# Performance work log

Hardware: AMD Instinct MI355X
Metric: run time of the kernel (lower is better)

## Reference

```python
import jax, jax.numpy as jnp
import numpy as np

B, N, C, H, K = 2, 4096, 256, 8, 32
D = C // H
EPS = 1e-5


def _ln(x, w, b):
    # LayerNorm over last axis
    m = x.mean(-1, keepdims=True)
    v = x.var(-1, keepdims=True)
    return (x - m) * jax.lax.rsqrt(v + EPS) * w + b


def setup_inputs() -> dict:
    key = jax.random.key(0)
    ks = jax.random.split(key, 16)
    s = 1.0 / np.sqrt(C)
    inp = {
        'xyz_A': jax.random.normal(ks[0], (B, N, 3), jnp.float32),
        'xyz_B': jax.random.normal(ks[1], (B, N, 3), jnp.float32),
        'featA': jax.random.normal(ks[2], (B, C, N), jnp.float32),
        'featB': jax.random.normal(ks[3], (B, C, N), jnp.float32),
        'ln_in_w': jnp.ones((C,), jnp.float32), 'ln_in_b': jnp.zeros((C,), jnp.float32),
        'wq': jax.random.normal(ks[4], (C, C), jnp.float32) * s, 'bq': jnp.zeros((C,), jnp.float32),
        'wk': jax.random.normal(ks[5], (C, C), jnp.float32) * s, 'bk': jnp.zeros((C,), jnp.float32),
        'wv': jax.random.normal(ks[6], (C, C), jnp.float32) * s, 'bv': jnp.zeros((C,), jnp.float32),
        'wqd': jax.random.normal(ks[7], (C, C), jnp.float32) * s, 'bqd': jnp.zeros((C,), jnp.float32),
        'wkd': jax.random.normal(ks[8], (C, C), jnp.float32) * s, 'bkd': jnp.zeros((C,), jnp.float32),
        'ln_sim_w': jnp.ones((C,), jnp.float32), 'ln_sim_b': jnp.zeros((C,), jnp.float32),
        'ln_dis_w': jnp.ones((C,), jnp.float32), 'ln_dis_b': jnp.zeros((C,), jnp.float32),
        'fus_w1': jax.random.normal(ks[9], (2 * C, 3 * C), jnp.float32) * (1.0 / np.sqrt(3 * C)),
        'bn_g': jnp.ones((2 * C,), jnp.float32), 'bn_b': jnp.zeros((2 * C,), jnp.float32),
        'fus_w2': jax.random.normal(ks[10], (C, 2 * C), jnp.float32) * (1.0 / np.sqrt(2 * C)),
        'fus_b2': jnp.zeros((C,), jnp.float32),
    }
    return inp


def reference(xyz_A, xyz_B, featA, featB, ln_in_w, ln_in_b,
              wq, bq, wk, bk, wv, bv, wqd, bqd, wkd, bkd,
              ln_sim_w, ln_sim_b, ln_dis_w, ln_dis_b,
              fus_w1, bn_g, bn_b, fus_w2, fus_b2):
    xA = featA.transpose(0, 2, 1)   # (B,N,C)
    xB = featB.transpose(0, 2, 1)   # (B,N,C)
    xA_n = _ln(xA, ln_in_w, ln_in_b)

    # KNN: nearest K points of xyz_B for each point in xyz_A
    d2 = (jnp.sum(xyz_A * xyz_A, -1)[:, :, None]
          + jnp.sum(xyz_B * xyz_B, -1)[:, None, :]
          - 2.0 * jnp.einsum('bnc,bmc->bnm', xyz_A, xyz_B))  # (B,N,N)
    _, knn_idx = jax.lax.top_k(-d2, K)  # (B,N,K)

    def proj(x, W, b):  # Conv1d k=1 on (B,N,C)
        return jnp.einsum('bnc,oc->bno', x, W) + b

    def heads(x):
        return x.reshape(B, N, H, D)

    q_s = heads(proj(xA_n, wq, bq))
    k_s = heads(proj(xB, wk, bk))
    v = heads(proj(xB, wv, bv))

    gather = jax.vmap(lambda f, i: f[i])  # (N,H,D),(N,K) -> (N,K,H,D)
    kN = gather(k_s, knn_idx)   # (B,N,K,H,D)
    vN = gather(v, knn_idx)     # (B,N,K,H,D)

    # similarity path: scaled dot-product over K neighbors
    sim = jnp.einsum('bnhd,bnkhd->bnhk', q_s, kN) / jnp.sqrt(jnp.float32(D))
    w_sim = jax.nn.softmax(sim, -1)
    ctx_s = jnp.einsum('bnhk,bnkhd->bnhd', w_sim, vN).reshape(B, N, C)
    ctx_s = _ln(ctx_s, ln_sim_w, ln_sim_b)

    # dissimilarity path: L2 distance scores
    q_d = heads(proj(xA_n, wqd, bqd))
    k_d = heads(proj(xB, wkd, bkd))
    kdN = gather(k_d, knn_idx)  # (B,N,K,H,D)
    diff = q_d[:, :, None] - kdN
    dist = jnp.sqrt(jnp.sum(diff * diff, -1)).transpose(0, 1, 3, 2)  # (B,N,H,K)
    w_dis = jax.nn.softmax(dist, -1)
    ctx_d = jnp.einsum('bnhk,bnkhd->bnhd', w_dis, vN).reshape(B, N, C)
    ctx_d = _ln(ctx_d, ln_dis_w, ln_dis_b)

    # fusion MLP (BN in eval mode: running mean 0, var 1)
    fused = jnp.concatenate([xA_n, ctx_s, ctx_d], -1)  # (B,N,3C)
    y = jnp.einsum('bnc,oc->bno', fused, fus_w1)
    y = y * jax.lax.rsqrt(jnp.float32(1.0 + EPS)) * bn_g + bn_b
    y = jax.nn.relu(y)
    y = jnp.einsum('bnc,oc->bno', y, fus_w2) + fus_b2

    out = y + xA  # residual (identity since in_channel == out_channel)
    return out.transpose(0, 2, 1)  # (B,C,N)
```

## Files before the change

kernel.cpp:

```cpp
#include <hip/hip_runtime.h>
#include <hip/hip_bf16.h>
#include <math.h>

#define B_ 2
#define N_ 4096
#define C_ 256
#define H_ 8
#define K_ 32
#define NP_ (B_*N_)
#define CAPW 256

typedef __attribute__((ext_vector_type(8))) short bf16x8;
typedef __attribute__((ext_vector_type(4))) float f32x4;
typedef __attribute__((ext_vector_type(4))) unsigned short ushort4_t;

__device__ __forceinline__ float bf2f(unsigned short v){
    union { unsigned int u; float f; } x; x.u = ((unsigned int)v) << 16; return x.f;
}
__device__ __forceinline__ unsigned short f2bf(float f){
    union { float f; unsigned int u; } x; x.f = f;
    return (unsigned short)((x.u + 0x7FFFu + ((x.u >> 16) & 1u)) >> 16);
}
__device__ __forceinline__ unsigned int mono(float f){
    union { float f; unsigned int u; } x; x.f = f;
    return x.u ^ (0x80000000u | (unsigned int)((int)x.u >> 31));
}
__device__ __forceinline__ void gload_lds16(const unsigned short* g, unsigned short* l){
    __builtin_amdgcn_global_load_lds(
        (const __attribute__((address_space(1))) unsigned int*)g,
        (__attribute__((address_space(3))) unsigned int*)l, 16, 0, 0);
}

__global__ __launch_bounds__(256) void k_pre(
    const float* __restrict__ s0, const float* __restrict__ s1,
    const float* __restrict__ s2, const float* __restrict__ s3,
    const float* __restrict__ s4, const float* __restrict__ s5,
    const float* __restrict__ s6, unsigned short* __restrict__ Wb,
    const float* __restrict__ xyzB, f32x4* __restrict__ PB,
    const float* __restrict__ xyzA, int* __restrict__ order,
    const float* __restrict__ featA, const float* __restrict__ lnw,
    const float* __restrict__ lnb, unsigned short* __restrict__ F,
    const float* __restrict__ featB, unsigned short* __restrict__ XBT)
{
    __shared__ __align__(16) char smem[35200];
    const int bid = blockIdx.x;
    const int tid = threadIdx.x;
    if (bid < 832){
        int i = (bid*256 + tid)*4;
        const float* s; int off;
        if (i < 327680){
            int seg = i >> 16;
            s = (seg==0)?s0:(seg==1)?s1:(seg==2)?s2:(seg==3)?s3:s4;
            off = i & 65535;
        } else if (i < 720896){
            s = s5; off = i - 327680;
        } else {
            s = s6; off = i - 720896;
        }
        f32x4 v = *(const f32x4*)(s + off);
        ushort4_t o;
        #pragma unroll
        for (int e = 0; e < 4; e++) o[e] = f2bf(v[e]);
        *(ushort4_t*)(Wb + i) = o;
    } else if (bid < 864){
        int i = (bid - 832)*256 + tid;
        float x = xyzB[i*3], y = xyzB[i*3+1], z = xyzB[i*3+2];
        f32x4 o;
        o[0] = -2.f*x; o[1] = -2.f*y; o[2] = -2.f*z;
        o[3] = x*x + y*y + z*z;
        PB[i] = o;
    } else if (bid < 866){
        unsigned int* hist = (unsigned int*)smem;
        unsigned int* wsum = (unsigned int*)(smem + 4096);
        const int b = bid - 864;
        const int wv = tid >> 6, lane = tid & 63;
        for (int i = tid; i < 1024; i += 256) hist[i] = 0u;
        __syncthreads();
        unsigned int code[16];
        #pragma unroll
        for (int i = 0; i < 16; i++){
            const int n = tid + i*256;
            const float* pp = xyzA + (size_t)((b<<12) + n)*3;
            int qx = (int)fminf(fmaxf((pp[0] + 5.f)*1.6f, 0.f), 15.f);
            int qy = (int)fminf(fmaxf((pp[1] + 5.f)*0.8f, 0.f), 7.f);
            int qz = (int)fminf(fmaxf((pp[2] + 5.f)*0.8f, 0.f), 7.f);
            unsigned int c = (unsigned int)((qx & 1) | ((qz & 1) << 1) | ((qy & 1) << 2)
                           | (((qx >> 1) & 1) << 3) | (((qz >> 1) & 1) << 4) | (((qy >> 1) & 1) << 5)
                           | (((qx >> 2) & 1) << 6) | (((qz >> 2) & 1) << 7) | (((qy >> 2) & 1) << 8)
                           | (((qx >> 3) & 1) << 9));
            code[i] = c;
            atomicAdd(&hist[c], 1u);
        }
        __syncthreads();
        unsigned int loc[4], t4 = 0;
        #pragma unroll
        for (int j = 0; j < 4; j++){ loc[j] = hist[tid*4 + j]; t4 += loc[j]; }
        unsigned int sc = t4;
        #pragma unroll
        for (int off = 1; off < 64; off <<= 1){
            unsigned int o = __shfl_up(sc, off, 64);
            if (lane >= off) sc += o;
        }
        if (lane == 63) wsum[wv] = sc;
        __syncthreads();
        unsigned int wb = 0;
        #pragma unroll
        for (int j = 0; j < 4; j++) if (j < wv) wb += wsum[j];
        unsigned int base = wb + sc - t4;
        #pragma unroll
        for (int j = 0; j < 4; j++){ hist[tid*4 + j] = base; base += loc[j]; }
        __syncthreads();
        #pragma unroll
        for (int i = 0; i < 16; i++){
            const int n = tid + i*256;
            unsigned int pos = atomicAdd(&hist[code[i]], 1u);
            order[(b<<12) + pos] = (b<<12) | n;
        }
    } else if (bid < 1122){
        float (*tile)[257] = (float(*)[257])smem;
        float (*ps)[32]    = (float(*)[32])(smem + 32896);
        float (*pq)[32]    = (float(*)[32])(smem + 33920);
        float (*st)[32]    = (float(*)[32])(smem + 34944);
        const int nx = tid & 31, cy = tid >> 5;
        const int pbase = (bid - 866) * 32;
        const int b = pbase >> 12, n0 = pbase & 4095;
        const float* sp = featA + (size_t)b*C_*N_ + n0;
        #pragma unroll 4
        for (int it = 0; it < 32; it++){
            int c = cy + it*8;
            tile[nx][c] = sp[(size_t)c*N_ + nx];
        }
        __syncthreads();
        {
            float s = 0.f, q = 0.f;
            #pragma unroll 8
            for (int i = 0; i < 32; i++){
                int cc = cy*32 + ((i + cy) & 31);
                float x = tile[nx][cc];
                s += x; q = fmaf(x, x, q);
            }
            ps[cy][nx] = s; pq[cy][nx] = q;
        }
        __syncthreads();
        if (tid < 32){
            float S = 0.f, Q = 0.f;
            #pragma unroll
            for (int j = 0; j < 8; j++){ S += ps[j][tid]; Q += pq[j][tid]; }
            float m = S*(1.f/256.f);
            float v = Q*(1.f/256.f) - m*m;
            st[0][tid] = m; st[1][tid] = rsqrtf(v + 1e-5f);
        }
        __syncthreads();
        const int p = pbase + nx;
        const float m = st[0][nx], r = st[1][nx];
        #pragma unroll
        for (int j = 0; j < 4; j++){
            bf16x8 ob;
            #pragma unroll
            for (int e = 0; e < 8; e++){
                int c = cy*32 + j*8 + e;
                ob[e] = (short)f2bf((tile[nx][c]-m)*r*lnw[c] + lnb[c]);
            }
            *(bf16x8*)(F + (size_t)p*768 + cy*32 + j*8) = ob;
        }
    } else {
        float (*tile)[65] = (float(*)[65])smem;
        const int idx = bid - 1122;
        const int x = idx & 63, y = (idx >> 6) & 3, z = idx >> 8;
        const int n0 = x*64, c0 = y*64;
        const int tx = tid & 63, ty = tid >> 6;
        const float* sp = featB + (size_t)z*C_*N_;
        #pragma unroll
        for (int i = 0; i < 16; i++){
            int cr = ty + i*4;
            tile[cr][tx] = sp[(size_t)(c0+cr)*N_ + n0 + tx];
        }
        __syncthreads();
        const int c = c0 + tx;
        #pragma unroll
        for (int i = 0; i < 16; i++){
            int nr = ty + i*4;
            int p = (z<<12) + n0 + nr;
            XBT[(size_t)p*256 + c] = f2bf(tile[tx][nr]);
        }
    }
}

__global__ __launch_bounds__(256) void k_knn(const float* __restrict__ xyzA,
        const f32x4* __restrict__ PB, int* __restrict__ knn){
    const int wv = threadIdx.x >> 6, lane = threadIdx.x & 63;
    const int p = blockIdx.x*4 + wv;
    const int b = p >> 12;
    const f32x4* pb = PB + ((size_t)b << 12);
    const float ax = xyzA[(size_t)p*3], ay = xyzA[(size_t)p*3+1], az = xyzA[(size_t)p*3+2];

    unsigned long long mn = ~0ull;
    #pragma unroll 8
    for (int i = 0; i < 64; i++){
        const int m = i*64 + lane;
        f32x4 c = pb[m];
        float d = fmaf(ax, c[0], fmaf(ay, c[1], fmaf(az, c[2], c[3])));
        unsigned long long key = (((unsigned long long)mono(d)) << 12) | (unsigned int)m;
        mn = key < mn ? key : mn;
    }
    unsigned int rk = 0;
    for (int j = 0; j < 64; j++){
        unsigned long long o = __shfl(mn, j, 64);
        rk += (o < mn) ? 1u : 0u;
    }
    unsigned long long sel = (rk == 31u) ? mn : ~0ull;
    #pragma unroll
    for (int off = 32; off; off >>= 1){
        unsigned long long o = __shfl_xor(sel, off, 64);
        sel = o < sel ? o : sel;
    }
    const unsigned long long v = sel;
    const unsigned int vhi = (unsigned int)(v >> 12);
    const unsigned int vlo = (unsigned int)(v & 0xFFFull);

    __shared__ unsigned long long cand[4][CAPW];
    __shared__ unsigned int cnt[4];
    if (lane == 0) cnt[wv] = 0u;
    #pragma unroll 8
    for (int i = 0; i < 64; i++){
        const int m = i*64 + lane;
        f32x4 c = pb[m];
        float d = fmaf(ax, c[0], fmaf(ay, c[1], fmaf(az, c[2], c[3])));
        unsigned int u = mono(d);
        if (u < vhi || (u == vhi && (unsigned int)m <= vlo)){
            unsigned int slot = atomicAdd(&cnt[wv], 1u);
            if (slot < CAPW)
                cand[wv][slot] = (((unsigned long long)u) << 12) | (unsigned int)m;
        }
    }
    const unsigned int C = cnt[wv];
    if (C <= CAPW){
        for (unsigned int i = lane; i < C; i += 64){
            unsigned long long mk = cand[wv][i];
            unsigned int rank = 0;
            for (unsigned int j = 0; j < C; j++) rank += (cand[wv][j] < mk) ? 1u : 0u;
            if (rank < K_) knn[(size_t)p*K_ + rank] = (int)(mk & 0xFFFull);
        }
    } else {
        unsigned long long last = 0ull;
        for (int it = 0; it < K_; it++){
            unsigned long long cm = ~0ull;
            #pragma unroll 4
            for (int i = 0; i < 64; i++){
                const int m = i*64 + lane;
                f32x4 c = pb[m];
                float d = fmaf(ax, c[0], fmaf(ay, c[1], fmaf(az, c[2], c[3])));
                unsigned long long key = (((unsigned long long)mono(d)) << 12) | (unsigned int)m;
                if (key > last && key < cm) cm = key;
            }
            #pragma unroll
            for (int off = 32; off; off >>= 1){
                unsigned long long o = __shfl_xor(cm, off, 64);
                cm = o < cm ? o : cm;
            }
            if (lane == 0) knn[(size_t)p*K_ + it] = (int)(cm & 0xFFFull);
            last = cm;
        }
    }
}

template<int MODE>
__device__ __forceinline__ void gemm_body(
    const unsigned short* __restrict__ X, int ldx,
    const unsigned short* __restrict__ W, int Kin,
    const float* __restrict__ e0, const float* __restrict__ e1, const float* __restrict__ e2,
    unsigned short* __restrict__ Y, int ldy,
    const float* __restrict__ resid, float* __restrict__ out,
    unsigned short (*As)[128*32], unsigned short (*Bs)[64*32], int bx, int by)
{
    const int tid = threadIdx.x, wid = tid >> 6, lane = tid & 63;
    const int lr = lane & 15, lg = lane >> 4;
    const int m0 = bx*128, n0 = by*64;
    const int lrow = lane >> 2, lcol = (lane & 3)*8;

    const unsigned short* Ag0 = X + (size_t)(m0 + wid*32 + lrow)*ldx + lcol;
    const unsigned short* Ag1 = X + (size_t)(m0 + wid*32 + 16 + lrow)*ldx + lcol;
    const unsigned short* Bg0 = W + (size_t)(n0 + wid*16 + lrow)*Kin + lcol;

    f32x4 acc[2][4] = {};
    const int NT = Kin >> 5;
    int buf = 0;
    gload_lds16(Ag0, &As[0][(wid*32)*32]);
    gload_lds16(Ag1, &As[0][(wid*32+16)*32]);
    gload_lds16(Bg0, &Bs[0][(wid*16)*32]);
    __syncthreads();
    for (int kt = 0; kt < NT; kt++){
        if (kt + 1 < NT){
            const int k = (kt+1)*32;
            gload_lds16(Ag0 + k, &As[buf^1][(wid*32)*32]);
            gload_lds16(Ag1 + k, &As[buf^1][(wid*32+16)*32]);
            gload_lds16(Bg0 + k, &Bs[buf^1][(wid*16)*32]);
        }
        bf16x8 a[2], b[4];
        #pragma unroll
        for (int mi = 0; mi < 2; mi++)
            a[mi] = *(const bf16x8*)&As[buf][(wid*32 + mi*16 + lr)*32 + lg*8];
        #pragma unroll
        for (int ni = 0; ni < 4; ni++)
            b[ni] = *(const bf16x8*)&Bs[buf][(ni*16 + lr)*32 + lg*8];
        #pragma unroll
        for (int mi = 0; mi < 2; mi++){
            #pragma unroll
            for (int ni = 0; ni < 4; ni++)
                acc[mi][ni] = __builtin_amdgcn_mfma_f32_16x16x32_bf16(a[mi], b[ni], acc[mi][ni], 0, 0, 0);
        }
        __syncthreads();
        buf ^= 1;
    }
    #pragma unroll
    for (int mi = 0; mi < 2; mi++){
        const int pbase = m0 + wid*32 + mi*16 + lg*4;
        #pragma unroll
        for (int ni = 0; ni < 4; ni++){
            const int o = n0 + ni*16 + lr;
            if (MODE == 0){
                const float* bp = (o < 256) ? e0 : ((o < 512) ? e1 : e2);
                float bias = bp[o & 255];
                #pragma unroll
                for (int r = 0; r < 4; r++)
                    Y[(size_t)(pbase + r)*ldy + o] = f2bf(acc[mi][ni][r] + bias);
            } else if (MODE == 1){
                float sc = e0[o] * 0.9999950000374997f;
                float sh = e1[o];
                #pragma unroll
                for (int r = 0; r < 4; r++){
                    float vv = fmaf(acc[mi][ni][r], sc, sh);
                    Y[(size_t)(pbase + r)*ldy + o] = f2bf(fmaxf(vv, 0.f));
                }
            } else {
                float bias = e0[o];
                const int b = pbase >> 12, nn = pbase & 4095;
                const size_t adr = ((size_t)b*C_ + o)*N_ + nn;
                f32x4 rv = *(const f32x4*)(resid + adr);
                f32x4 ov;
                #pragma unroll
                for (int r = 0; r < 4; r++) ov[r] = acc[mi][ni][r] + bias + rv[r];
                *(f32x4*)(out + adr) = ov;
            }
        }
    }
}

__global__ __launch_bounds__(256) void k_proj(
    const unsigned short* __restrict__ F, const unsigned short* __restrict__ XBT,
    const unsigned short* __restrict__ WQcat, const unsigned short* __restrict__ WKVD,
    const float* __restrict__ bq, const float* __restrict__ bqd,
    const float* __restrict__ bk, const float* __restrict__ bv, const float* __restrict__ bkd,
    unsigned short* __restrict__ QQ, unsigned short* __restrict__ KVD)
{
    __shared__ __align__(16) unsigned short As[2][128*32];
    __shared__ __align__(16) unsigned short Bs[2][64*32];
    if (blockIdx.y < 8)
        gemm_body<0>(F, 768, WQcat, 256, bq, bqd, nullptr, QQ, 512, nullptr, nullptr,
                     As, Bs, blockIdx.x, blockIdx.y);
    else
        gemm_body<0>(XBT, 256, WKVD, 256, bk, bv, bkd, KVD, 768, nullptr, nullptr,
                     As, Bs, blockIdx.x, blockIdx.y - 8);
}

template<int MODE>
__global__ __launch_bounds__(256) void k_gemm(
    const unsigned short* __restrict__ X, int ldx,
    const unsigned short* __restrict__ W, int Kin,
    const float* __restrict__ e0, const float* __restrict__ e1, const float* __restrict__ e2,
    unsigned short* __restrict__ Y, int ldy,
    const float* __restrict__ resid, float* __restrict__ out)
{
    __shared__ __align__(16) unsigned short As[2][128*32];
    __shared__ __align__(16) unsigned short Bs[2][64*32];
    gemm_body<MODE>(X, ldx, W, Kin, e0, e1, e2, Y, ldy, resid, out,
                    As, Bs, blockIdx.x, blockIdx.y);
}

__global__ __launch_bounds__(128) void k_attn(
    const unsigned short* __restrict__ QQ, const unsigned short* __restrict__ KVD,
    const int* __restrict__ KNN, const int* __restrict__ order,
    const float* __restrict__ lnsw, const float* __restrict__ lnsb,
    const float* __restrict__ lndw, const float* __restrict__ lndb,
    unsigned short* __restrict__ F)
{
    __shared__ int   idx_l[2][32];
    __shared__ float part_l[2][4];

    const int tid = threadIdx.x;
    const int wh = tid >> 6, lane = tid & 63;
    const int bid = blockIdx.x;
    const int xcd = bid & 7, ib = bid >> 3;
    const int batch = xcd & 1, quarter = xcd >> 1;
    const int p = order[(batch << 12) + quarter*1024 + ib];
    const int b = batch;

    if (lane < 32) idx_l[wh][lane] = KNN[(size_t)p*K_ + lane];

    const int tq = lane >> 4, c = lane & 15;

    float qsf[8], qdf[8];
    {
        const unsigned short* qrow = QQ + (size_t)p*512 + wh*128 + c*8;
        bf16x8 qs8 = *(const bf16x8*)(qrow);
        bf16x8 qd8 = *(const bf16x8*)(qrow + 256);
        #pragma unroll
        for (int e = 0; e < 8; e++){
            qsf[e] = bf2f((unsigned short)qs8[e]);
            qdf[e] = bf2f((unsigned short)qd8[e]);
        }
    }
    const unsigned short* KB = KVD + (size_t)(b << 12)*768;
    int nbt[8];
    #pragma unroll
    for (int i = 0; i < 8; i++) nbt[i] = idx_l[wh][tq + i*4];

    float s[8];
    {
        bf16x8 kx[8];
        #pragma unroll
        for (int i = 0; i < 8; i++)
            kx[i] = *(const bf16x8*)(KB + (size_t)nbt[i]*768 + wh*128 + c*8);
        #pragma unroll
        for (int i = 0; i < 8; i++){
            float a = 0.f;
            #pragma unroll
            for (int e = 0; e < 8; e++)
                a = fmaf(qsf[e], bf2f((unsigned short)kx[i][e]), a);
            s[i] = a;
        }
    }
    float t[8];
    {
        bf16x8 dx[8];
        #pragma unroll
        for (int i = 0; i < 8; i++)
            dx[i] = *(const bf16x8*)(KB + (size_t)nbt[i]*768 + 512 + wh*128 + c*8);
        #pragma unroll
        for (int i = 0; i < 8; i++){
            float a = 0.f;
            #pragma unroll
            for (int e = 0; e < 8; e++){
                float df = qdf[e] - bf2f((unsigned short)dx[i][e]);
                a = fmaf(df, df, a);
            }
            t[i] = a;
        }
    }
    bf16x8 vx[8];
    #pragma unroll
    for (int i = 0; i < 8; i++)
        vx[i] = *(const bf16x8*)(KB + (size_t)nbt[i]*768 + 256 + wh*128 + c*8);

    #pragma unroll
    for (int i = 0; i < 8; i++){
        s[i] += __shfl_xor(s[i], 1, 64); s[i] += __shfl_xor(s[i], 2, 64);
        t[i] += __shfl_xor(t[i], 1, 64); t[i] += __shfl_xor(t[i], 2, 64);
    }
    float sim[8], dist[8];
    #pragma unroll
    for (int i = 0; i < 8; i++){
        sim[i]  = s[i] * 0.17677669529663687f;
        dist[i] = sqrtf(t[i]);
    }
    float m1 = sim[0], m2 = dist[0];
    #pragma unroll
    for (int i = 1; i < 8; i++){ m1 = fmaxf(m1, sim[i]); m2 = fmaxf(m2, dist[i]); }
    m1 = fmaxf(m1, __shfl_xor(m1, 16, 64)); m1 = fmaxf(m1, __shfl_xor(m1, 32, 64));
    m2 = fmaxf(m2, __shfl_xor(m2, 16, 64)); m2 = fmaxf(m2, __shfl_xor(m2, 32, 64));
    float e1[8], e2[8], s1 = 0.f, s2 = 0.f;
    #pragma unroll
    for (int i = 0; i < 8; i++){
        e1[i] = __expf(sim[i] - m1);  s1 += e1[i];
        e2[i] = __expf(dist[i] - m2); s2 += e2[i];
    }
    s1 += __shfl_xor(s1, 16, 64); s1 += __shfl_xor(s1, 32, 64);
    s2 += __shfl_xor(s2, 16, 64); s2 += __shfl_xor(s2, 32, 64);
    const float r1i = 1.f / s1, r2i = 1.f / s2;

    float cs[8] = {0,0,0,0,0,0,0,0}, cd[8] = {0,0,0,0,0,0,0,0};
    #pragma unroll
    for (int i = 0; i < 8; i++){
        const float w1 = e1[i] * r1i;
        const float w2 = e2[i] * r2i;
        #pragma unroll
        for (int e = 0; e < 8; e++){
            float vf = bf2f((unsigned short)vx[i][e]);
            cs[e] = fmaf(w1, vf, cs[e]);
            cd[e] = fmaf(w2, vf, cd[e]);
        }
    }
    #pragma unroll
    for (int e = 0; e < 8; e++){
        cs[e] += __shfl_xor(cs[e], 16, 64); cs[e] += __shfl_xor(cs[e], 32, 64);
        cd[e] += __shfl_xor(cd[e], 16, 64); cd[e] += __shfl_xor(cd[e], 32, 64);
    }
    float s1n = 0.f, q1n = 0.f, s2n = 0.f, q2n = 0.f;
    #pragma unroll
    for (int e = 0; e < 8; e++){
        s1n += cs[e]; q1n = fmaf(cs[e], cs[e], q1n);
        s2n += cd[e]; q2n = fmaf(cd[e], cd[e], q2n);
    }
    #pragma unroll
    for (int off = 1; off < 16; off <<= 1){
        s1n += __shfl_xor(s1n, off, 64); q1n += __shfl_xor(q1n, off, 64);
        s2n += __shfl_xor(s2n, off, 64); q2n += __shfl_xor(q2n, off, 64);
    }
    if (lane == 0){
        part_l[wh][0] = s1n; part_l[wh][1] = q1n;
        part_l[wh][2] = s2n; part_l[wh][3] = q2n;
    }
    __syncthreads();
    const float S1 = s1n + part_l[wh^1][0];
    const float Q1 = q1n + part_l[wh^1][1];
    const float S2 = s2n + part_l[wh^1][2];
    const float Q2 = q2n + part_l[wh^1][3];
    const float mm1 = S1*(1.f/256.f), mm2 = S2*(1.f/256.f);
    const float rr1 = rsqrtf(Q1*(1.f/256.f) - mm1*mm1 + 1e-5f);
    const float rr2 = rsqrtf(Q2*(1.f/256.f) - mm2*mm2 + 1e-5f);

    if (tq == 0){
        bf16x8 ob;
        #pragma unroll
        for (int e = 0; e < 8; e++){
            const int cg = wh*128 + c*8 + e;
            ob[e] = (short)f2bf((cs[e]-mm1)*rr1*lnsw[cg] + lnsb[cg]);
        }
        *(bf16x8*)(F + (size_t)p*768 + 256 + wh*128 + c*8) = ob;
    } else if (tq == 1){
        bf16x8 ob;
        #pragma unroll
        for (int e = 0; e < 8; e++){
            const int cg = wh*128 + c*8 + e;
            ob[e] = (short)f2bf((cd[e]-mm2)*rr2*lndw[cg] + lndb[cg]);
        }
        *(bf16x8*)(F + (size_t)p*768 + 512 + wh*128 + c*8) = ob;
    }
}

extern "C" void kernel_launch(void* const* d_in, const int* in_sizes, int n_in,
                              void* d_out, int out_size, void* d_ws, size_t ws_size,
                              hipStream_t stream)
{
    const float* xyzA   = (const float*)d_in[0];
    const float* xyzB   = (const float*)d_in[1];
    const float* featA  = (const float*)d_in[2];
    const float* featB  = (const float*)d_in[3];
    const float* ln_in_w= (const float*)d_in[4];
    const float* ln_in_b= (const float*)d_in[5];
    const float* wq  = (const float*)d_in[6];
    const float* bq  = (const float*)d_in[7];
    const float* wk  = (const float*)d_in[8];
    const float* bk  = (const float*)d_in[9];
    const float* wv  = (const float*)d_in[10];
    const float* bv  = (const float*)d_in[11];
    const float* wqd = (const float*)d_in[12];
    const float* bqd = (const float*)d_in[13];
    const float* wkd = (const float*)d_in[14];
    const float* bkd = (const float*)d_in[15];
    const float* lnsw = (const float*)d_in[16];
    const float* lnsb = (const float*)d_in[17];
    const float* lndw = (const float*)d_in[18];
    const float* lndb = (const float*)d_in[19];
    const float* fw1 = (const float*)d_in[20];
    const float* bng = (const float*)d_in[21];
    const float* bnb = (const float*)d_in[22];
    const float* fw2 = (const float*)d_in[23];
    const float* fb2 = (const float*)d_in[24];
    float* out = (float*)d_out;
    char* ws = (char*)d_ws;

    unsigned short* F    = (unsigned short*)(ws + 0);
    unsigned short* XBT  = (unsigned short*)(ws + 12582912);
    unsigned short* QQ   = (unsigned short*)(ws + 16777216);
    unsigned short* KVD  = (unsigned short*)(ws + 25165824);
    unsigned short* Y1   = (unsigned short*)(ws + 37748736);
    f32x4*          PB   = (f32x4*)(ws + 37748736);
    int*            KNNi = (int*)(ws + 46137344);
    int*            ORD  = (int*)(ws + 47185920);
    unsigned short* Wb   = (unsigned short*)(ws + 47251456);
    unsigned short* WQcat = Wb;
    unsigned short* WKVD  = Wb + 131072;
    unsigned short* W1b   = Wb + 327680;
    unsigned short* W2b   = Wb + 720896;

    k_pre<<<1634, 256, 0, stream>>>(wq, wqd, wk, wv, wkd, fw1, fw2, Wb,
                                    xyzB, PB, xyzA, ORD,
                                    featA, ln_in_w, ln_in_b, F, featB, XBT);
    k_knn<<<2048, 256, 0, stream>>>(xyzA, PB, KNNi);

    k_proj<<<dim3(64,20), 256, 0, stream>>>(F, XBT, WQcat, WKVD, bq, bqd, bk, bv, bkd, QQ, KVD);

    k_attn<<<8192, 128, 0, stream>>>(QQ, KVD, KNNi, ORD, lnsw, lnsb, lndw, lndb, F);

    k_gemm<1><<<dim3(64,8), 256, 0, stream>>>(F,  768, W1b, 768, bng, bnb, nullptr, Y1, 512, nullptr, nullptr);
    k_gemm<2><<<dim3(64,4), 256, 0, stream>>>(Y1, 512, W2b, 512, fb2, nullptr, nullptr, nullptr, 0, featA, out);
}
```

Baseline: 129.1 us.

## Process two query points per wavefront in KNN to reuse candidate loads

The KNN kernel now has each wavefront handle two query points, so every loaded B-point coordinate feeds two distance computations and the grid is halved. The first min pass tracks float distance plus index instead of packed 64-bit keys, and the candidate filter compares floats against an unmono'd threshold. This cuts global loads and 64-bit compares per query. In exchange it doubles shared candidate storage, adds register pressure, and changes how ties at the threshold are handled, which can let more candidates through the filter.

After: 127.9 us. Within noise of the previous version (-0.9%).

```diff
diff --git a/kernel.cpp b/kernel.cpp
--- a/kernel.cpp
+++ b/kernel.cpp
@@ -24,6 +24,11 @@
 __device__ __forceinline__ unsigned int mono(float f){
     union { float f; unsigned int u; } x; x.f = f;
     return x.u ^ (0x80000000u | (unsigned int)((int)x.u >> 31));
+}
+__device__ __forceinline__ float unmono(unsigned int u){
+    union { unsigned int u; float f; } x;
+    x.u = (u & 0x80000000u) ? (u ^ 0x80000000u) : ~u;
+    return x.f;
 }
 __device__ __forceinline__ void gload_lds16(const unsigned short* g, unsigned short* l){
     __builtin_amdgcn_global_load_lds(
@@ -189,77 +194,125 @@
 __global__ __launch_bounds__(256) void k_knn(const float* __restrict__ xyzA,
         const f32x4* __restrict__ PB, int* __restrict__ knn){
     const int wv = threadIdx.x >> 6, lane = threadIdx.x & 63;
-    const int p = blockIdx.x*4 + wv;
-    const int b = p >> 12;
+    const int q0 = blockIdx.x*8 + wv*2;
+    const int b = q0 >> 12;
     const f32x4* pb = PB + ((size_t)b << 12);
-    const float ax = xyzA[(size_t)p*3], ay = xyzA[(size_t)p*3+1], az = xyzA[(size_t)p*3+2];
-
-    unsigned long long mn = ~0ull;
+    const float ax0 = xyzA[(size_t)q0*3],     ay0 = xyzA[(size_t)q0*3+1],     az0 = xyzA[(size_t)q0*3+2];
+    const float ax1 = xyzA[(size_t)(q0+1)*3], ay1 = xyzA[(size_t)(q0+1)*3+1], az1 = xyzA[(size_t)(q0+1)*3+2];
+
+    float dm0 = 3.4e38f, dm1 = 3.4e38f;
+    int   mi0 = 0, mi1 = 0;
     #pragma unroll 8
     for (int i = 0; i < 64; i++){
         const int m = i*64 + lane;
         f32x4 c = pb[m];
-        float d = fmaf(ax, c[0], fmaf(ay, c[1], fmaf(az, c[2], c[3])));
-        unsigned long long key = (((unsigned long long)mono(d)) << 12) | (unsigned int)m;
-        mn = key < mn ? key : mn;
-    }
-    unsigned int rk = 0;
+        float d0 = fmaf(ax0, c[0], fmaf(ay0, c[1], fmaf(az0, c[2], c[3])));
+        float d1 = fmaf(ax1, c[0], fmaf(ay1, c[1], fmaf(az1, c[2], c[3])));
+        if (d0 < dm0){ dm0 = d0; mi0 = m; }
+        if (d1 < dm1){ dm1 = d1; mi1 = m; }
+    }
+    const unsigned long long key0 = (((unsigned long long)mono(dm0)) << 12) | (unsigned int)mi0;
+    const unsigned long long key1 = (((unsigned long long)mono(dm1)) << 12) | (unsigned int)mi1;
+    unsigned int rk0 = 0, rk1 = 0;
     for (int j = 0; j < 64; j++){
-        unsigned long long o = __shfl(mn, j, 64);
-        rk += (o < mn) ? 1u : 0u;
-    }
-    unsigned long long sel = (rk == 31u) ? mn : ~0ull;
+        unsigned long long o0 = __shfl(key0, j, 64);
+        unsigned long long o1 = __shfl(key1, j, 64);
+        rk0 += (o0 < key0) ? 1u : 0u;
+        rk1 += (o1 < key1) ? 1u : 0u;
+    }
+    unsigned long long sel0 = (rk0 == 31u) ? key0 : ~0ull;
+    unsigned long long sel1 = (rk1 == 31u) ? key1 : ~0ull;
     #pragma unroll
     for (int off = 32; off; off >>= 1){
-        unsigned long long o = __shfl_xor(sel, off, 64);
-        sel = o < sel ? o : sel;
-    }
-    const unsigned long long v = sel;
-    const unsigned int vhi = (unsigned int)(v >> 12);
-    const unsigned int vlo = (unsigned int)(v & 0xFFFull);
-
-    __shared__ unsigned long long cand[4][CAPW];
-    __shared__ unsigned int cnt[4];
-    if (lane == 0) cnt[wv] = 0u;
-    #pragma unroll 8
+        unsigned long long o0 = __shfl_xor(sel0, off, 64);
+        unsigned long long o1 = __shfl_xor(sel1, off, 64);
+        sel0 = o0 < sel0 ? o0 : sel0;
+        sel1 = o1 < sel1 ? o1 : sel1;
+    }
+    const float vf0 = unmono((unsigned int)(sel0 >> 12));
+    const float vf1 = unmono((unsigned int)(sel1 >> 12));
+
+    __shared__ unsigned long long cand[8][CAPW];
+    __shared__ unsigned int cnt[8];
+    const int s0 = wv*2, s1 = wv*2 + 1;
+    if (lane == 0){ cnt[s0] = 0u; cnt[s1] = 0u; }
+    #pragma unroll 4
     for (int i = 0; i < 64; i++){
         const int m = i*64 + lane;
         f32x4 c = pb[m];
-        float d = fmaf(ax, c[0], fmaf(ay, c[1], fmaf(az, c[2], c[3])));
-        unsigned int u = mono(d);
-        if (u < vhi || (u == vhi && (unsigned int)m <= vlo)){
-            unsigned int slot = atomicAdd(&cnt[wv], 1u);
+        float d0 = fmaf(ax0, c[0], fmaf(ay0, c[1], fmaf(az0, c[2], c[3])));
+        float d1 = fmaf(ax1, c[0], fmaf(ay1, c[1], fmaf(az1, c[2], c[3])));
+        if (d0 <= vf0){
+            unsigned int slot = atomicAdd(&cnt[s0], 1u);
             if (slot < CAPW)
-                cand[wv][slot] = (((unsigned long long)u) << 12) | (unsigned int)m;
-        }
-    }
-    const unsigned int C = cnt[wv];
-    if (C <= CAPW){
-        for (unsigned int i = lane; i < C; i += 64){
-            unsigned long long mk = cand[wv][i];
-            unsigned int rank = 0;
-            for (unsigned int j = 0; j < C; j++) rank += (cand[wv][j] < mk) ? 1u : 0u;
-            if (rank < K_) knn[(size_t)p*K_ + rank] = (int)(mk & 0xFFFull);
-        }
-    } else {
-        unsigned long long last = 0ull;
-        for (int it = 0; it < K_; it++){
-            unsigned long long cm = ~0ull;
-            #pragma unroll 4
-            for (int i = 0; i < 64; i++){
-                const int m = i*64 + lane;
-                f32x4 c = pb[m];
-                float d = fmaf(ax, c[0], fmaf(ay, c[1], fmaf(az, c[2], c[3])));
-                unsigned long long key = (((unsigned long long)mono(d)) << 12) | (unsigned int)m;
-                if (key > last && key < cm) cm = key;
-            }
-            #pragma unroll
-            for (int off = 32; off; off >>= 1){
-                unsigned long long o = __shfl_xor(cm, off, 64);
-                cm = o < cm ? o : cm;
-            }
-            if (lane == 0) knn[(size_t)p*K_ + it] = (int)(cm & 0xFFFull);
-            last = cm;
+                cand[s0][slot] = (((unsigned long long)mono(d0)) << 12) | (unsigned int)m;
+        }
+        if (d1 <= vf1){
+            unsigned int slot = atomicAdd(&cnt[s1], 1u);
+            if (slot < CAPW)
+                cand[s1][slot] = (((unsigned long long)mono(d1)) << 12) | (unsigned int)m;
+        }
+    }
+    {
+        const unsigned int C = cnt[s0];
+        if (C <= CAPW){
+            for (unsigned int i = lane; i < C; i += 64){
+                unsigned long long mk = cand[s0][i];
+                unsigned int rank = 0;
+                for (unsigned int j = 0; j < C; j++) rank += (cand[s0][j] < mk) ? 1u : 0u;
+                if (rank < K_) knn[(size_t)q0*K_ + rank] = (int)(mk & 0xFFFull);
+            }
+        } else {
+            unsigned long long last = 0ull;
+            for (int it = 0; it < K_; it++){
+                unsigned long long cm = ~0ull;
+                #pragma unroll 4
+                for (int i = 0; i < 64; i++){
+                    const int m = i*64 + lane;
+                    f32x4 c = pb[m];
+                    float d = fmaf(ax0, c[0], fmaf(ay0, c[1], fmaf(az0, c[2], c[3])));
+                    unsigned long long key = (((unsigned long long)mono(d)) << 12) | (unsigned int)m;
+                    if (key > last && key < cm) cm = key;
+                }
+                #pragma unroll
+                for (int off = 32; off; off >>= 1){
+                    unsigned long long o = __shfl_xor(cm, off, 64);
+                    cm = o < cm ? o : cm;
+                }
+                if (lane == 0) knn[(size_t)q0*K_ + it] = (int)(cm & 0xFFFull);
+                last = cm;
+            }
+        }
+    }
+    {
+        const unsigned int C = cnt[s1];
+        if (C <= CAPW){
+            for (unsigned int i = lane; i < C; i += 64){
+                unsigned long long mk = cand[s1][i];
+                unsigned int rank = 0;
+                for (unsigned int j = 0; j < C; j++) rank += (cand[s1][j] < mk) ? 1u : 0u;
+                if (rank < K_) knn[(size_t)(q0+1)*K_ + rank] = (int)(mk & 0xFFFull);
+            }
+        } else {
+            unsigned long long last = 0ull;
+            for (int it = 0; it < K_; it++){
+                unsigned long long cm = ~0ull;
+                #pragma unroll 4
+                for (int i = 0; i < 64; i++){
+                    const int m = i*64 + lane;
+                    f32x4 c = pb[m];
+                    float d = fmaf(ax1, c[0], fmaf(ay1, c[1], fmaf(az1, c[2], c[3])));
+                    unsigned long long key = (((unsigned long long)mono(d)) << 12) | (unsigned int)m;
+                    if (key > last && key < cm) cm = key;
+                }
+                #pragma unroll
+                for (int off = 32; off; off >>= 1){
+                    unsigned long long o = __shfl_xor(cm, off, 64);
+                    cm = o < cm ? o : cm;
+                }
+                if (lane == 0) knn[(size_t)(q0+1)*K_ + it] = (int)(cm & 0xFFFull);
+                last = cm;
+            }
         }
     }
 }
@@ -587,7 +640,7 @@
     k_pre<<<1634, 256, 0, stream>>>(wq, wqd, wk, wv, wkd, fw1, fw2, Wb,
                                     xyzB, PB, xyzA, ORD,
                                     featA, ln_in_w, ln_in_b, F, featB, XBT);
-    k_knn<<<2048, 256, 0, stream>>>(xyzA, PB, KNNi);
+    k_knn<<<1024, 256, 0, stream>>>(xyzA, PB, KNNi);
 
     k_proj<<<dim3(64,20), 256, 0, stream>>>(F, XBT, WQcat, WKVD, bq, bqd, bk, bv, bkd, QQ, KVD);
 
```

## Process four query points per wavefront in KNN to reuse loaded candidates

Applied to the files above, without the earlier changes.

Each wavefront of the KNN kernel now handles four query points, so every candidate point loaded from global memory is reused for four distance evaluations. The grid shrinks from 2048 to 512 blocks and the shared candidate buffer becomes 16 slabs with capacity cut from 256 to 128. The threshold filter now compares float distances against an un-mapped threshold instead of packed integer keys. The risks are fewer blocks in flight (less latency hiding), more register pressure, and more frequent fallback to the slow iterative path if a candidate list overflows 128.

Measured after the change: 138.5 us. 7.3% more time.

```diff
diff --git a/kernel.cpp b/kernel.cpp
--- a/kernel.cpp
+++ b/kernel.cpp
@@ -8,7 +8,7 @@
 #define H_ 8
 #define K_ 32
 #define NP_ (B_*N_)
-#define CAPW 256
+#define CAPW 128
 
 typedef __attribute__((ext_vector_type(8))) short bf16x8;
 typedef __attribute__((ext_vector_type(4))) float f32x4;
@@ -24,6 +24,11 @@
 __device__ __forceinline__ unsigned int mono(float f){
     union { float f; unsigned int u; } x; x.f = f;
     return x.u ^ (0x80000000u | (unsigned int)((int)x.u >> 31));
+}
+__device__ __forceinline__ float unmono(unsigned int u){
+    union { unsigned int u; float f; } x;
+    x.u = (u & 0x80000000u) ? (u ^ 0x80000000u) : ~u;
+    return x.f;
 }
 __device__ __forceinline__ void gload_lds16(const unsigned short* g, unsigned short* l){
     __builtin_amdgcn_global_load_lds(
@@ -189,77 +194,104 @@
 __global__ __launch_bounds__(256) void k_knn(const float* __restrict__ xyzA,
         const f32x4* __restrict__ PB, int* __restrict__ knn){
     const int wv = threadIdx.x >> 6, lane = threadIdx.x & 63;
-    const int p = blockIdx.x*4 + wv;
-    const int b = p >> 12;
+    const int q0 = blockIdx.x*16 + wv*4;
+    const int b = q0 >> 12;
     const f32x4* pb = PB + ((size_t)b << 12);
-    const float ax = xyzA[(size_t)p*3], ay = xyzA[(size_t)p*3+1], az = xyzA[(size_t)p*3+2];
-
-    unsigned long long mn = ~0ull;
-    #pragma unroll 8
+    float axq[4], ayq[4], azq[4];
+    #pragma unroll
+    for (int qq = 0; qq < 4; qq++){
+        axq[qq] = xyzA[(size_t)(q0+qq)*3];
+        ayq[qq] = xyzA[(size_t)(q0+qq)*3+1];
+        azq[qq] = xyzA[(size_t)(q0+qq)*3+2];
+    }
+
+    float dm[4] = {3.4e38f, 3.4e38f, 3.4e38f, 3.4e38f};
+    int   mi[4] = {0,0,0,0};
+    #pragma unroll 4
     for (int i = 0; i < 64; i++){
         const int m = i*64 + lane;
         f32x4 c = pb[m];
-        float d = fmaf(ax, c[0], fmaf(ay, c[1], fmaf(az, c[2], c[3])));
-        unsigned long long key = (((unsigned long long)mono(d)) << 12) | (unsigned int)m;
-        mn = key < mn ? key : mn;
-    }
-    unsigned int rk = 0;
+        #pragma unroll
+        for (int qq = 0; qq < 4; qq++){
+            float d = fmaf(axq[qq], c[0], fmaf(ayq[qq], c[1], fmaf(azq[qq], c[2], c[3])));
+            if (d < dm[qq]){ dm[qq] = d; mi[qq] = m; }
+        }
+    }
+    unsigned long long key[4];
+    #pragma unroll
+    for (int qq = 0; qq < 4; qq++)
+        key[qq] = (((unsigned long long)mono(dm[qq])) << 12) | (unsigned int)mi[qq];
+    unsigned int rk[4] = {0,0,0,0};
     for (int j = 0; j < 64; j++){
-        unsigned long long o = __shfl(mn, j, 64);
-        rk += (o < mn) ? 1u : 0u;
-    }
-    unsigned long long sel = (rk == 31u) ? mn : ~0ull;
+        #pragma unroll
+        for (int qq = 0; qq < 4; qq++){
+            unsigned long long o = __shfl(key[qq], j, 64);
+            rk[qq] += (o < key[qq]) ? 1u : 0u;
+        }
+    }
+    unsigned long long sel[4];
+    #pragma unroll
+    for (int qq = 0; qq < 4; qq++) sel[qq] = (rk[qq] == 31u) ? key[qq] : ~0ull;
     #pragma unroll
     for (int off = 32; off; off >>= 1){
-        unsigned long long o = __shfl_xor(sel, off, 64);
-        sel = o < sel ? o : sel;
-    }
-    const unsigned long long v = sel;
-    const unsigned int vhi = (unsigned int)(v >> 12);
-    const unsigned int vlo = (unsigned int)(v & 0xFFFull);
-
-    __shared__ unsigned long long cand[4][CAPW];
-    __shared__ unsigned int cnt[4];
-    if (lane == 0) cnt[wv] = 0u;
-    #pragma unroll 8
+        #pragma unroll
+        for (int qq = 0; qq < 4; qq++){
+            unsigned long long o = __shfl_xor(sel[qq], off, 64);
+            sel[qq] = o < sel[qq] ? o : sel[qq];
+        }
+    }
+    float vf[4];
+    #pragma unroll
+    for (int qq = 0; qq < 4; qq++) vf[qq] = unmono((unsigned int)(sel[qq] >> 12));
+
+    __shared__ unsigned long long cand[16][CAPW];
+    __shared__ unsigned int cnt[16];
+    if (lane < 4) cnt[wv*4 + lane] = 0u;
+    #pragma unroll 4
     for (int i = 0; i < 64; i++){
         const int m = i*64 + lane;
         f32x4 c = pb[m];
-        float d = fmaf(ax, c[0], fmaf(ay, c[1], fmaf(az, c[2], c[3])));
-        unsigned int u = mono(d);
-        if (u < vhi || (u == vhi && (unsigned int)m <= vlo)){
-            unsigned int slot = atomicAdd(&cnt[wv], 1u);
-            if (slot < CAPW)
-                cand[wv][slot] = (((unsigned long long)u) << 12) | (unsigned int)m;
-        }
-    }
-    const unsigned int C = cnt[wv];
-    if (C <= CAPW){
-        for (unsigned int i = lane; i < C; i += 64){
-            unsigned long long mk = cand[wv][i];
-            unsigned int rank = 0;
-            for (unsigned int j = 0; j < C; j++) rank += (cand[wv][j] < mk) ? 1u : 0u;
-            if (rank < K_) knn[(size_t)p*K_ + rank] = (int)(mk & 0xFFFull);
-        }
-    } else {
-        unsigned long long last = 0ull;
-        for (int it = 0; it < K_; it++){
-            unsigned long long cm = ~0ull;
-            #pragma unroll 4
-            for (int i = 0; i < 64; i++){
-                const int m = i*64 + lane;
-                f32x4 c = pb[m];
-                float d = fmaf(ax, c[0], fmaf(ay, c[1], fmaf(az, c[2], c[3])));
-                unsigned long long key = (((unsigned long long)mono(d)) << 12) | (unsigned int)m;
-                if (key > last && key < cm) cm = key;
+        #pragma unroll
+        for (int qq = 0; qq < 4; qq++){
+            float d = fmaf(axq[qq], c[0], fmaf(ayq[qq], c[1], fmaf(azq[qq], c[2], c[3])));
+            if (d <= vf[qq]){
+                unsigned int slot = atomicAdd(&cnt[wv*4 + qq], 1u);
+                if (slot < CAPW)
+                    cand[wv*4 + qq][slot] = (((unsigned long long)mono(d)) << 12) | (unsigned int)m;
             }
-            #pragma unroll
-            for (int off = 32; off; off >>= 1){
-                unsigned long long o = __shfl_xor(cm, off, 64);
-                cm = o < cm ? o : cm;
+        }
+    }
+    #pragma unroll
+    for (int qq = 0; qq < 4; qq++){
+        const int slab = wv*4 + qq;
+        const unsigned int C = cnt[slab];
+        if (C <= CAPW){
+            for (unsigned int i = lane; i < C; i += 64){
+                unsigned long long mk = cand[slab][i];
+                unsigned int rank = 0;
+                for (unsigned int j = 0; j < C; j++) rank += (cand[slab][j] < mk) ? 1u : 0u;
+                if (rank < K_) knn[(size_t)(q0+qq)*K_ + rank] = (int)(mk & 0xFFFull);
             }
-            if (lane == 0) knn[(size_t)p*K_ + it] = (int)(cm & 0xFFFull);
-            last = cm;
+        } else {
+            unsigned long long last = 0ull;
+            for (int it = 0; it < K_; it++){
+                unsigned long long cm = ~0ull;
+                #pragma unroll 4
+                for (int i = 0; i < 64; i++){
+                    const int m = i*64 + lane;
+                    f32x4 c = pb[m];
+                    float d = fmaf(axq[qq], c[0], fmaf(ayq[qq], c[1], fmaf(azq[qq], c[2], c[3])));
+                    unsigned long long kk2 = (((unsigned long long)mono(d)) << 12) | (unsigned int)m;
+                    if (kk2 > last && kk2 < cm) cm = kk2;
+                }
+                #pragma unroll
+                for (int off = 32; off; off >>= 1){
+                    unsigned long long o = __shfl_xor(cm, off, 64);
+                    cm = o < cm ? o : cm;
+                }
+                if (lane == 0) knn[(size_t)(q0+qq)*K_ + it] = (int)(cm & 0xFFFull);
+                last = cm;
+            }
         }
     }
 }
@@ -587,7 +619,7 @@
     k_pre<<<1634, 256, 0, stream>>>(wq, wqd, wk, wv, wkd, fw1, fw2, Wb,
                                     xyzB, PB, xyzA, ORD,
                                     featA, ln_in_w, ln_in_b, F, featB, XBT);
-    k_knn<<<2048, 256, 0, stream>>>(xyzA, PB, KNNi);
+    k_knn<<<512, 256, 0, stream>>>(xyzA, PB, KNNi);
 
     k_proj<<<dim3(64,20), 256, 0, stream>>>(F, XBT, WQcat, WKVD, bq, bqd, bk, bv, bkd, QQ, KVD);
 
```
